# Performance work log

Hardware: AMD Instinct MI355X
Metric: run time of the kernel (lower is better)

The kernel has to match this reference:

```python
import jax, jax.numpy as jnp
import numpy as np

# batches, users-per-batch (max_user_num), servers-per-batch (max_server_num), dims
B, U, S, DU, DS, H = 64, 256, 64, 16, 16, 256
DEG_S, DEG_U = 8, 16
NU, NS = B * U, B * S
IN_DIM = U * DU + S * DS  # 5120


def setup_inputs() -> dict:
    key = jax.random.key(0)
    ks = jax.random.split(key, 12)
    x_user = jax.random.normal(ks[0], (NU, DU), jnp.float32)
    x_server = jax.random.normal(ks[1], (NS, DS), jnp.float32)
    # within-batch edges: user u in batch u//U connects to servers/users of same batch
    src_u2s = jnp.repeat(jnp.arange(NU), DEG_S)
    dst_u2s = (src_u2s // U) * S + jax.random.randint(ks[2], (NU * DEG_S,), 0, S)
    src_u2u = jnp.repeat(jnp.arange(NU), DEG_U)
    dst_u2u = (src_u2u // U) * U + jax.random.randint(ks[3], (NU * DEG_U,), 0, U)

    def lin(k, i, o):
        return jax.random.normal(k, (i, o), jnp.float32) * 0.02

    params = dict(
        oW1=lin(ks[4], IN_DIM, H), ob1=jnp.zeros((H,), jnp.float32),
        oW2=lin(ks[5], H, H), ob2=jnp.zeros((H,), jnp.float32),
        oW3=lin(ks[6], H, 2), ob3=jnp.zeros((2,), jnp.float32),
        sW1=lin(ks[7], IN_DIM, H), sb1=jnp.zeros((H,), jnp.float32),
        sW2=lin(ks[8], H, H), sb2=jnp.zeros((H,), jnp.float32),
        sW3=lin(ks[9], H, S), sb3=jnp.zeros((S,), jnp.float32),
    )
    return dict(x_user=x_user, x_server=x_server,
                src_u2s=src_u2s, dst_u2s=dst_u2s,
                src_u2u=src_u2u, dst_u2u=dst_u2u, **params)


def _mlp3(x, W1, b1, W2, b2, W3, b3):
    h = jax.nn.relu(x @ W1 + b1)
    h = jax.nn.sigmoid(h @ W2 + b2)
    return h @ W3 + b3


def reference(x_user, x_server, src_u2s, dst_u2s, src_u2u, dst_u2u,
              oW1, ob1, oW2, ob2, oW3, ob3, sW1, sb1, sW2, sb2, sW3, sb3):
    # scatter neighbor features into per-user dense observation slots
    # (edges are within-batch, so dst % S / dst % U is the local slot index,
    #  identical to the original global-offset scatter + batch mask)
    server_obs = (jnp.zeros((NU, S, DS), x_server.dtype)
                  .at[src_u2s, dst_u2s % S].set(x_server[dst_u2s]))
    user_obs = (jnp.zeros((NU, U, DU), x_user.dtype)
                .at[src_u2u, dst_u2u % U].set(x_user[dst_u2u]))
    feats = jnp.concatenate([server_obs.reshape(B, U, S * DS),
                             user_obs.reshape(B, U, U * DU)], axis=-1)  # [B,U,IN_DIM]
    offloading_probs = jax.nn.softmax(
        _mlp3(feats, oW1, ob1, oW2, ob2, oW3, ob3), axis=-1)  # [B,U,2]
    sel_logits = _mlp3(feats, sW1, sb1, sW2, sb2, sW3, sb3)   # [B,U,S]
    # -inf mask: 0 only at (user, server) pairs connected by a u2s edge
    non_probs = (jnp.full((NU, S), -jnp.inf, jnp.float32)
                 .at[src_u2s, dst_u2s % S].set(0.0)
                 .reshape(B, U, S))
    selection_probs = jax.nn.softmax(sel_logits + non_probs, axis=-1)
    return offloading_probs, selection_probs
```

## Files before the change

kernel.cpp:

```cpp
#include <hip/hip_runtime.h>
#include <hip/hip_bf16.h>
#include <math.h>
#include <cstdint>

#define NUSER 16384
#define BB    64
#define UU    256
#define SSLOT 64
#define HD    256
#define KTOT  320
#define DEGS  8
#define DEGU  16

typedef __attribute__((ext_vector_type(8))) short short8;
typedef __attribute__((ext_vector_type(4))) float f32x4;

static __device__ __forceinline__ __hip_bfloat16 f2b(float x) { return __float2bfloat16(x); }
static __device__ __forceinline__ unsigned pack2(float x, float y) {
  union { __hip_bfloat16 h[2]; unsigned u; } cv;
  cv.h[0] = f2b(x); cv.h[1] = f2b(y);
  return cv.u;
}

__global__ __launch_bounds__(256) void k_prep_pq(
    const int* __restrict__ dst_u2s, const int* __restrict__ dst_u2u,
    const float* __restrict__ oW2, const float* __restrict__ sW2,
    const float* __restrict__ sW3,
    const float* __restrict__ xu, const float* __restrict__ xs,
    const float* __restrict__ oW1, const float* __restrict__ sW1,
    unsigned long long* __restrict__ connS, unsigned* __restrict__ MSUW,
    __hip_bfloat16* __restrict__ W2T_o, __hip_bfloat16* __restrict__ W2T_s,
    __hip_bfloat16* __restrict__ W3T_s,
    __hip_bfloat16* __restrict__ P_o, __hip_bfloat16* __restrict__ P_s,
    __hip_bfloat16* __restrict__ Q_o, __hip_bfloat16* __restrict__ Q_s) {
  const int t = threadIdx.x;
  if (blockIdx.y == 0) {
    const int blk = blockIdx.x;
    if (blk < 64) {
      const int u = blk * 256 + t;
      unsigned long long ms = 0ull;
      #pragma unroll
      for (int i = 0; i < DEGS; ++i) ms |= 1ull << (dst_u2s[u * DEGS + i] & 63);
      connS[u] = ms;
      unsigned long long m0 = 0, m1 = 0, m2 = 0, m3 = 0;
      #pragma unroll
      for (int i = 0; i < DEGU; ++i) {
        int slot = dst_u2u[u * DEGU + i] & 255;
        unsigned long long bit = 1ull << (slot & 63);
        int w = slot >> 6;
        if (w == 0) m0 |= bit; else if (w == 1) m1 |= bit;
        else if (w == 2) m2 |= bit; else m3 |= bit;
      }
      unsigned* mw = MSUW + (size_t)u * 10;
      uint2* mw2 = (uint2*)mw;
      mw2[0] = make_uint2((unsigned)ms, (unsigned)(ms >> 32));
      mw2[1] = make_uint2((unsigned)m0, (unsigned)(m0 >> 32));
      mw2[2] = make_uint2((unsigned)m1, (unsigned)(m1 >> 32));
      mw2[3] = make_uint2((unsigned)m2, (unsigned)(m2 >> 32));
      mw2[4] = make_uint2((unsigned)m3, (unsigned)(m3 >> 32));
    } else {
      const int n = blk - 64;
      W2T_o[n * HD + t] = f2b(oW2[t * HD + n]);
      W2T_s[n * HD + t] = f2b(sW2[t * HD + n]);
      if (n < SSLOT) W3T_s[n * HD + t] = f2b(sW3[t * SSLOT + n]);
    }
    return;
  }
  const int wg = blockIdx.x;
  const int b0 = (blockIdx.y - 1) * 8;
  __shared__ float lx[8 * 16];
  const bool isS = wg < SSLOT;
  const int slot = isS ? wg : wg - SSLOT;
  if (t < 8 * 16) {
    int b = b0 + (t >> 4), d = t & 15;
    lx[t] = isS ? xs[(b * SSLOT + slot) * 16 + d] : xu[(b * UU + slot) * 16 + d];
  }
  __syncthreads();
  float wo[16], wsv[16];
  const int rbase = isS ? slot * 16 : SSLOT * 16 + slot * 16;
  #pragma unroll
  for (int d = 0; d < 16; ++d) {
    wo[d] = oW1[(rbase + d) * HD + t];
    wsv[d] = sW1[(rbase + d) * HD + t];
  }
  __hip_bfloat16* Ro = isS ? P_o : Q_o;
  __hip_bfloat16* Rs = isS ? P_s : Q_s;
  const int rows = isS ? SSLOT : UU;
  #pragma unroll
  for (int bi = 0; bi < 8; ++bi) {
    float ao = 0.f, as = 0.f;
    #pragma unroll
    for (int q = 0; q < 4; ++q) {
      float4 x4 = *(const float4*)&lx[bi * 16 + q * 4];
      ao = fmaf(x4.x, wo[q*4+0], ao); as = fmaf(x4.x, wsv[q*4+0], as);
      ao = fmaf(x4.y, wo[q*4+1], ao); as = fmaf(x4.y, wsv[q*4+1], as);
      ao = fmaf(x4.z, wo[q*4+2], ao); as = fmaf(x4.z, wsv[q*4+2], as);
      ao = fmaf(x4.w, wo[q*4+3], ao); as = fmaf(x4.w, wsv[q*4+3], as);
    }
    Ro[((b0 + bi) * rows + slot) * HD + t] = f2b(ao);
    Rs[((b0 + bi) * rows + slot) * HD + t] = f2b(as);
  }
}

__global__ __launch_bounds__(256) void k_tr(
    const __hip_bfloat16* __restrict__ P_o, const __hip_bfloat16* __restrict__ P_s,
    const __hip_bfloat16* __restrict__ Q_o, const __hip_bfloat16* __restrict__ Q_s,
    __hip_bfloat16* __restrict__ PQT_o, __hip_bfloat16* __restrict__ PQT_s) {
  const int b = blockIdx.x, mlp = blockIdx.y, nc = blockIdx.z;
  const int n0 = nc * 64;
  const int t = threadIdx.x;
  const __hip_bfloat16* P = mlp ? P_s : P_o;
  const __hip_bfloat16* Q = mlp ? Q_s : Q_o;
  __hip_bfloat16* PQT = mlp ? PQT_s : PQT_o;
  __shared__ __align__(16) short lds[64 * 72];
  for (int kt = 0; kt < 5; ++kt) {
    const __hip_bfloat16* src = (kt == 0) ? (P + (size_t)(b * SSLOT) * HD)
                                          : (Q + (size_t)(b * UU + (kt - 1) * 64) * HD);
    const int kout = (kt == 0) ? 0 : 64 + (kt - 1) * 64;
    #pragma unroll
    for (int i = 0; i < 2; ++i) {
      int c = t + i * 256;
      int row = c >> 3, cc = c & 7;
      *(short8*)&lds[row * 72 + cc * 8] =
          *(const short8*)(src + (size_t)row * HD + n0 + cc * 8);
    }
    __syncthreads();
    #pragma unroll
    for (int i = 0; i < 2; ++i) {
      int c = t + i * 256;
      int nrow = c >> 3, kc = c & 7;
      short8 v;
      #pragma unroll
      for (int e = 0; e < 8; ++e) v[e] = lds[(kc * 8 + e) * 72 + nrow];
      *(short8*)(PQT + (size_t)(b * 256 + n0 + nrow) * KTOT + kout + kc * 8) = v;
    }
    __syncthreads();
  }
}

__global__ __launch_bounds__(256) void k_h1(
    const unsigned* __restrict__ MSUW,
    const __hip_bfloat16* __restrict__ PQT_o, const __hip_bfloat16* __restrict__ PQT_s,
    const float* __restrict__ ob1, const float* __restrict__ sb1,
    __hip_bfloat16* __restrict__ h1o, __hip_bfloat16* __restrict__ h1s) {
  const int b = blockIdx.x >> 1, uh = blockIdx.x & 1;
  const int mlp = blockIdx.y, nh = blockIdx.z;
  const int n0 = nh * 128;
  const int t = threadIdx.x;
  const __hip_bfloat16* PQT = mlp ? PQT_s : PQT_o;
  const float* b1 = mlp ? sb1 : ob1;
  __hip_bfloat16* h1 = mlp ? h1s : h1o;

  __shared__ __align__(16) char smem[48128];
  short* pan = (short*)smem;
  unsigned* mskL = (unsigned*)(smem + 43008);

  {
    const unsigned* g = MSUW + (size_t)(b * 256 + uh * 128) * 10;
    #pragma unroll
    for (int i = 0; i < 5; ++i) mskL[t + 256 * i] = g[t + 256 * i];
  }
  const int lane = t & 63, w = t >> 6;
  const int lo = lane & 15, hi = lane >> 4;
  f32x4 acc[2][8] = {};
  for (int kc = 0; kc < 2; ++kc) {
    if (kc) __syncthreads();
    {
      const int r = t >> 1, c4 = t & 1;
      const __hip_bfloat16* src = PQT + (size_t)(b * 256 + n0 + r) * KTOT + kc * 160;
      #pragma unroll
      for (int i = 0; i < 10; ++i) {
        int cc = c4 + 2 * i;
        *(short8*)&pan[r * 168 + cc * 8] = *(const short8*)(src + cc * 8);
      }
    }
    __syncthreads();
    #pragma unroll
    for (int kt2 = 0; kt2 < 5; ++kt2) {
      const int kt = kc * 5 + kt2;
      short8 af[2], bf[8];
      #pragma unroll
      for (int rb = 0; rb < 2; ++rb) {
        int lu = w * 32 + rb * 16 + lo;
        unsigned m = mskL[lu * 10 + kt];
        unsigned by = (m >> (hi * 8)) & 0xFFu;
        union { unsigned u[4]; short8 s; } cv;
        cv.u[0] = ((by & 1u)  ? 0x3F80u : 0u) | ((by & 2u)   ? 0x3F800000u : 0u);
        cv.u[1] = ((by & 4u)  ? 0x3F80u : 0u) | ((by & 8u)   ? 0x3F800000u : 0u);
        cv.u[2] = ((by & 16u) ? 0x3F80u : 0u) | ((by & 32u)  ? 0x3F800000u : 0u);
        cv.u[3] = ((by & 64u) ? 0x3F80u : 0u) | ((by & 128u) ? 0x3F800000u : 0u);
        af[rb] = cv.s;
      }
      #pragma unroll
      for (int cb = 0; cb < 8; ++cb) {
        int n = cb * 16 + lo;
        bf[cb] = *(const short8*)&pan[n * 168 + (kt2 * 4 + hi) * 8];
      }
      #pragma unroll
      for (int rb = 0; rb < 2; ++rb)
        #pragma unroll
        for (int cb = 0; cb < 8; ++cb)
          acc[rb][cb] = __builtin_amdgcn_mfma_f32_16x16x32_bf16(af[rb], bf[cb], acc[rb][cb], 0, 0, 0);
    }
  }
  #pragma unroll
  for (int cb = 0; cb < 8; ++cb) {
    int n = cb * 16 + lo;
    float bv = b1[n0 + n];
    #pragma unroll
    for (int rb = 0; rb < 2; ++rb) {
      #pragma unroll
      for (int j = 0; j < 4; ++j) {
        int u = b * 256 + uh * 128 + w * 32 + rb * 16 + hi * 4 + j;
        h1[(size_t)u * HD + n0 + n] = f2b(fmaxf(acc[rb][cb][j] + bv, 0.f));
      }
    }
  }
}

__global__ __launch_bounds__(256) void k_heads(
    const __hip_bfloat16* __restrict__ h1o, const __hip_bfloat16* __restrict__ h1s,
    const __hip_bfloat16* __restrict__ W2T_o, const __hip_bfloat16* __restrict__ W2T_s,
    const float* __restrict__ ob2, const float* __restrict__ sb2,
    const float* __restrict__ oW3, const float* __restrict__ ob3,
    const __hip_bfloat16* __restrict__ W3T_s, const float* __restrict__ sb3,
    const unsigned long long* __restrict__ connS,
    float* __restrict__ out) {
  const int mlp = blockIdx.y;
  const int x = blockIdx.x;
  const int blk = (x & 7) * 32 + (x >> 3);
  const int u0 = blk * 64;
  const int t = threadIdx.x, lane = t & 63, wid = t >> 6;
  const int lo = lane & 15, hi = lane >> 4;

  const __hip_bfloat16* A   = mlp ? h1s : h1o;
  const __hip_bfloat16* W2T = mlp ? W2T_s : W2T_o;
  const float* b2 = mlp ? sb2 : ob2;

  __shared__ __align__(16) char lds[32768 + 36864];
  short* As = (short*)lds;
  short* Bs = (short*)(lds + 32768);
  float* part = (float*)lds;

  #pragma unroll
  for (int i = 0; i < 8; ++i) {
    int c = t + i * 256;
    int row = c >> 5, cc = c & 31;
    *(short8*)&As[row * 256 + (cc ^ (row & 7)) * 8] =
        *(const short8*)(A + (size_t)(u0 + row) * HD + cc * 8);
  }
  __syncthreads();

  f32x4 acc2[4][4] = {};
  for (int ks = 0; ks < 8; ++ks) {
    if (ks) __syncthreads();
    #pragma unroll
    for (int i = 0; i < 4; ++i) {
      int c = t + i * 256;
      int n = c >> 2, kc = c & 3;
      *(short8*)&Bs[n * 72 + kc * 8] =
          *(const short8*)(W2T + (size_t)n * HD + ks * 32 + kc * 8);
    }
    __syncthreads();
    short8 af[4], bf[4];
    #pragma unroll
    for (int rb = 0; rb < 4; ++rb) {
      int row = rb * 16 + lo;
      int ca = ks * 4 + hi;
      af[rb] = *(const short8*)&As[row * 256 + (ca ^ (row & 7)) * 8];
    }
    #pragma unroll
    for (int cb = 0; cb < 4; ++cb) {
      int n = wid * 64 + cb * 16 + lo;
      bf[cb] = *(const short8*)&Bs[n * 72 + hi * 8];
    }
    #pragma unroll
    for (int rb = 0; rb < 4; ++rb)
      #pragma unroll
      for (int cb = 0; cb < 4; ++cb)
        acc2[rb][cb] = __builtin_amdgcn_mfma_f32_16x16x32_bf16(af[rb], bf[cb], acc2[rb][cb], 0, 0, 0);
  }
  __syncthreads();

  if (mlp == 0) {
    float p0[4][4] = {}, p1[4][4] = {};
    #pragma unroll
    for (int cb = 0; cb < 4; ++cb) {
      int n = wid * 64 + cb * 16 + lo;
      float bs = b2[n], w0 = oW3[2 * n], w1 = oW3[2 * n + 1];
      #pragma unroll
      for (int rb = 0; rb < 4; ++rb)
        #pragma unroll
        for (int j = 0; j < 4; ++j) {
          float sig = 1.0f / (1.0f + __expf(-(acc2[rb][cb][j] + bs)));
          p0[rb][j] = fmaf(sig, w0, p0[rb][j]);
          p1[rb][j] = fmaf(sig, w1, p1[rb][j]);
        }
    }
    #pragma unroll
    for (int rb = 0; rb < 4; ++rb)
      #pragma unroll
      for (int j = 0; j < 4; ++j) {
        #pragma unroll
        for (int off = 1; off < 16; off <<= 1) {
          p0[rb][j] += __shfl_xor(p0[rb][j], off, 64);
          p1[rb][j] += __shfl_xor(p1[rb][j], off, 64);
        }
        if (lo == 0) {
          int row = rb * 16 + hi * 4 + j;
          part[wid * 128 + row * 2 + 0] = p0[rb][j];
          part[wid * 128 + row * 2 + 1] = p1[rb][j];
        }
      }
    __syncthreads();
    if (t < 64) {
      float q0 = part[t * 2] + part[128 + t * 2] + part[256 + t * 2] + part[384 + t * 2] + ob3[0];
      float q1 = part[t * 2 + 1] + part[128 + t * 2 + 1] + part[256 + t * 2 + 1] + part[384 + t * 2 + 1] + ob3[1];
      float m2 = fmaxf(q0, q1);
      float e0 = __expf(q0 - m2), e1 = __expf(q1 - m2);
      float iv = 1.0f / (e0 + e1);
      float2 r; r.x = e0 * iv; r.y = e1 * iv;
      *(float2*)(out + (size_t)(u0 + t) * 2) = r;
    }
  } else {
    short* sel = As;
    #pragma unroll
    for (int cb = 0; cb < 4; ++cb) {
      int n = wid * 64 + cb * 16 + lo;
      float bs = b2[n];
      #pragma unroll
      for (int rb = 0; rb < 4; ++rb)
        #pragma unroll
        for (int j = 0; j < 4; ++j) {
          int row = rb * 16 + hi * 4 + j;
          float sig = 1.0f / (1.0f + __expf(-(acc2[rb][cb][j] + bs)));
          sel[row * 256 + ((n >> 3) ^ (row & 7)) * 8 + (n & 7)] = (short)pack2(sig, 0.f);
        }
    }
    __syncthreads();
    f32x4 acc3[4] = {};
    #pragma unroll
    for (int ks = 0; ks < 8; ++ks) {
      int row = wid * 16 + lo;
      int ca = ks * 4 + hi;
      short8 af = *(const short8*)&sel[row * 256 + (ca ^ (row & 7)) * 8];
      #pragma unroll
      for (int cb = 0; cb < 4; ++cb) {
        short8 bf = *(const short8*)(W3T_s + (size_t)(cb * 16 + lo) * HD + ks * 32 + hi * 8);
        acc3[cb] = __builtin_amdgcn_mfma_f32_16x16x32_bf16(af, bf, acc3[cb], 0, 0, 0);
      }
    }
    float sb3n[4];
    #pragma unroll
    for (int cb = 0; cb < 4; ++cb) sb3n[cb] = sb3[cb * 16 + lo];
    const int ubase = u0 + wid * 16 + hi * 4;
    #pragma unroll
    for (int j = 0; j < 4; ++j) {
      unsigned long long m = connS[ubase + j];
      float v[4]; bool ok[4];
      float mx = -INFINITY;
      #pragma unroll
      for (int cb = 0; cb < 4; ++cb) {
        int n = cb * 16 + lo;
        ok[cb] = (m >> n) & 1ull;
        v[cb] = ok[cb] ? (acc3[cb][j] + sb3n[cb]) : -INFINITY;
        mx = fmaxf(mx, v[cb]);
      }
      #pragma unroll
      for (int off = 1; off < 16; off <<= 1) mx = fmaxf(mx, __shfl_xor(mx, off, 64));
      float e[4], ssum = 0.f;
      #pragma unroll
      for (int cb = 0; cb < 4; ++cb) {
        e[cb] = ok[cb] ? __expf(v[cb] - mx) : 0.f;
        ssum += e[cb];
      }
      #pragma unroll
      for (int off = 1; off < 16; off <<= 1) ssum += __shfl_xor(ssum, off, 64);
      float iv = 1.0f / ssum;
      #pragma unroll
      for (int cb = 0; cb < 4; ++cb) {
        int n = cb * 16 + lo;
        out[(size_t)NUSER * 2 + (size_t)(ubase + j) * SSLOT + n] = e[cb] * iv;
      }
    }
  }
}

extern "C" void kernel_launch(void* const* d_in, const int* in_sizes, int n_in,
                              void* d_out, int out_size, void* d_ws, size_t ws_size,
                              hipStream_t stream) {
  const float* x_user   = (const float*)d_in[0];
  const float* x_server = (const float*)d_in[1];
  const int*   dst_u2s  = (const int*)d_in[3];
  const int*   dst_u2u  = (const int*)d_in[5];
  const float* oW1 = (const float*)d_in[6];
  const float* ob1 = (const float*)d_in[7];
  const float* oW2 = (const float*)d_in[8];
  const float* ob2 = (const float*)d_in[9];
  const float* oW3 = (const float*)d_in[10];
  const float* ob3 = (const float*)d_in[11];
  const float* sW1 = (const float*)d_in[12];
  const float* sb1 = (const float*)d_in[13];
  const float* sW2 = (const float*)d_in[14];
  const float* sb2 = (const float*)d_in[15];
  const float* sW3 = (const float*)d_in[16];
  const float* sb3 = (const float*)d_in[17];

  char* ws = (char*)d_ws;
  unsigned long long* connS = (unsigned long long*)(ws + 0);
  unsigned*       MSUW  = (unsigned*)(ws + 131072);
  __hip_bfloat16* P_o  = (__hip_bfloat16*)(ws + 786432);
  __hip_bfloat16* P_s  = (__hip_bfloat16*)(ws + 2883584);
  __hip_bfloat16* Q_o  = (__hip_bfloat16*)(ws + 4980736);
  __hip_bfloat16* Q_s  = (__hip_bfloat16*)(ws + 13369344);
  __hip_bfloat16* PQT_o = (__hip_bfloat16*)(ws + 21757952);
  __hip_bfloat16* PQT_s = (__hip_bfloat16*)(ws + 32243712);
  __hip_bfloat16* h1o  = (__hip_bfloat16*)(ws + 42729472);
  __hip_bfloat16* h1s  = (__hip_bfloat16*)(ws + 51118080);
  __hip_bfloat16* W2T_o = (__hip_bfloat16*)(ws + 59506688);
  __hip_bfloat16* W2T_s = (__hip_bfloat16*)(ws + 59637760);
  __hip_bfloat16* W3T_s = (__hip_bfloat16*)(ws + 59768832);
  float* out = (float*)d_out;

  k_prep_pq<<<dim3(320, 9), 256, 0, stream>>>(
      dst_u2s, dst_u2u, oW2, sW2, sW3, x_user, x_server, oW1, sW1,
      connS, MSUW, W2T_o, W2T_s, W3T_s, P_o, P_s, Q_o, Q_s);
  k_tr<<<dim3(64, 2, 4), 256, 0, stream>>>(P_o, P_s, Q_o, Q_s, PQT_o, PQT_s);
  k_h1<<<dim3(128, 2, 2), 256, 0, stream>>>(MSUW, PQT_o, PQT_s, ob1, sb1, h1o, h1s);
  k_heads<<<dim3(256, 2), 256, 0, stream>>>(h1o, h1s, W2T_o, W2T_s, ob2, sb2,
                                            oW3, ob3, W3T_s, sb3, connS, out);
}
```

Baseline: 58.02 us.

## Pre-swizzle W2/W3 into MFMA fragment order and load B directly from global

The prep kernel now writes the second- and third-layer weights in a layout that matches the MFMA B-operand fragment per lane. The heads kernel then loads each B fragment with one contiguous 16-byte read from global or L2, instead of staging W2 tiles through LDS with two barriers per k-step. This removes the LDS staging, the barriers and about 36KB of shared memory per block, which may allow higher occupancy. In exchange every wave reads its weights from L2 rather than sharing them through LDS.

```diff
diff --git a/kernel.cpp b/kernel.cpp
--- a/kernel.cpp
+++ b/kernel.cpp
@@ -29,8 +29,8 @@
     const float* __restrict__ xu, const float* __restrict__ xs,
     const float* __restrict__ oW1, const float* __restrict__ sW1,
     unsigned long long* __restrict__ connS, unsigned* __restrict__ MSUW,
-    __hip_bfloat16* __restrict__ W2T_o, __hip_bfloat16* __restrict__ W2T_s,
-    __hip_bfloat16* __restrict__ W3T_s,
+    __hip_bfloat16* __restrict__ W2F_o, __hip_bfloat16* __restrict__ W2F_s,
+    __hip_bfloat16* __restrict__ W3F_s,
     __hip_bfloat16* __restrict__ P_o, __hip_bfloat16* __restrict__ P_s,
     __hip_bfloat16* __restrict__ Q_o, __hip_bfloat16* __restrict__ Q_s) {
   const int t = threadIdx.x;
@@ -58,11 +58,21 @@
       mw2[2] = make_uint2((unsigned)m1, (unsigned)(m1 >> 32));
       mw2[3] = make_uint2((unsigned)m2, (unsigned)(m2 >> 32));
       mw2[4] = make_uint2((unsigned)m3, (unsigned)(m3 >> 32));
+      {
+        const int n = blk;
+        const int ks = t >> 5, hi = (t >> 3) & 3, e = t & 7;
+        const int lane = hi * 16 + (n & 15);
+        const size_t idx = (size_t)((((n >> 4) * 8 + ks) * 64 + lane)) * 8 + e;
+        W3F_s[idx] = f2b(sW3[(ks * 32 + hi * 8 + e) * SSLOT + n]);
+      }
     } else {
       const int n = blk - 64;
-      W2T_o[n * HD + t] = f2b(oW2[t * HD + n]);
-      W2T_s[n * HD + t] = f2b(sW2[t * HD + n]);
-      if (n < SSLOT) W3T_s[n * HD + t] = f2b(sW3[t * SSLOT + n]);
+      const int ks = t >> 5, hi = (t >> 3) & 3, e = t & 7;
+      const int lane = hi * 16 + (n & 15);
+      const size_t idx = (size_t)((((n >> 4) * 8 + ks) * 64 + lane)) * 8 + e;
+      const int k = ks * 32 + hi * 8 + e;
+      W2F_o[idx] = f2b(oW2[k * HD + n]);
+      W2F_s[idx] = f2b(sW2[k * HD + n]);
     }
     return;
   }
@@ -220,10 +230,10 @@
 
 __global__ __launch_bounds__(256) void k_heads(
     const __hip_bfloat16* __restrict__ h1o, const __hip_bfloat16* __restrict__ h1s,
-    const __hip_bfloat16* __restrict__ W2T_o, const __hip_bfloat16* __restrict__ W2T_s,
+    const __hip_bfloat16* __restrict__ W2F_o, const __hip_bfloat16* __restrict__ W2F_s,
     const float* __restrict__ ob2, const float* __restrict__ sb2,
     const float* __restrict__ oW3, const float* __restrict__ ob3,
-    const __hip_bfloat16* __restrict__ W3T_s, const float* __restrict__ sb3,
+    const __hip_bfloat16* __restrict__ W3F_s, const float* __restrict__ sb3,
     const unsigned long long* __restrict__ connS,
     float* __restrict__ out) {
   const int mlp = blockIdx.y;
@@ -234,13 +244,12 @@
   const int lo = lane & 15, hi = lane >> 4;
 
   const __hip_bfloat16* A   = mlp ? h1s : h1o;
-  const __hip_bfloat16* W2T = mlp ? W2T_s : W2T_o;
+  const __hip_bfloat16* W2F = mlp ? W2F_s : W2F_o;
   const float* b2 = mlp ? sb2 : ob2;
 
-  __shared__ __align__(16) char lds[32768 + 36864];
+  __shared__ __align__(16) char lds[32768 + 2048];
   short* As = (short*)lds;
-  short* Bs = (short*)(lds + 32768);
-  float* part = (float*)lds;
+  float* part = (float*)(lds + 32768);
 
   #pragma unroll
   for (int i = 0; i < 8; ++i) {
@@ -252,16 +261,8 @@
   __syncthreads();
 
   f32x4 acc2[4][4] = {};
+  #pragma unroll
   for (int ks = 0; ks < 8; ++ks) {
-    if (ks) __syncthreads();
-    #pragma unroll
-    for (int i = 0; i < 4; ++i) {
-      int c = t + i * 256;
-      int n = c >> 2, kc = c & 3;
-      *(short8*)&Bs[n * 72 + kc * 8] =
-          *(const short8*)(W2T + (size_t)n * HD + ks * 32 + kc * 8);
-    }
-    __syncthreads();
     short8 af[4], bf[4];
     #pragma unroll
     for (int rb = 0; rb < 4; ++rb) {
@@ -271,8 +272,7 @@
     }
     #pragma unroll
     for (int cb = 0; cb < 4; ++cb) {
-      int n = wid * 64 + cb * 16 + lo;
-      bf[cb] = *(const short8*)&Bs[n * 72 + hi * 8];
+      bf[cb] = *(const short8*)(W2F + (size_t)((((wid * 4 + cb) * 8 + ks) * 64 + lane)) * 8);
     }
     #pragma unroll
     for (int rb = 0; rb < 4; ++rb)
@@ -346,7 +346,7 @@
       short8 af = *(const short8*)&sel[row * 256 + (ca ^ (row & 7)) * 8];
       #pragma unroll
       for (int cb = 0; cb < 4; ++cb) {
-        short8 bf = *(const short8*)(W3T_s + (size_t)(cb * 16 + lo) * HD + ks * 32 + hi * 8);
+        short8 bf = *(const short8*)(W3F_s + (size_t)(((cb * 8 + ks) * 64 + lane)) * 8);
         acc3[cb] = __builtin_amdgcn_mfma_f32_16x16x32_bf16(af, bf, acc3[cb], 0, 0, 0);
       }
     }
@@ -417,16 +417,16 @@
   __hip_bfloat16* PQT_s = (__hip_bfloat16*)(ws + 32243712);
   __hip_bfloat16* h1o  = (__hip_bfloat16*)(ws + 42729472);
   __hip_bfloat16* h1s  = (__hip_bfloat16*)(ws + 51118080);
-  __hip_bfloat16* W2T_o = (__hip_bfloat16*)(ws + 59506688);
-  __hip_bfloat16* W2T_s = (__hip_bfloat16*)(ws + 59637760);
-  __hip_bfloat16* W3T_s = (__hip_bfloat16*)(ws + 59768832);
+  __hip_bfloat16* W2F_o = (__hip_bfloat16*)(ws + 59506688);
+  __hip_bfloat16* W2F_s = (__hip_bfloat16*)(ws + 59637760);
+  __hip_bfloat16* W3F_s = (__hip_bfloat16*)(ws + 59768832);
   float* out = (float*)d_out;
 
   k_prep_pq<<<dim3(320, 9), 256, 0, stream>>>(
       dst_u2s, dst_u2u, oW2, sW2, sW3, x_user, x_server, oW1, sW1,
-      connS, MSUW, W2T_o, W2T_s, W3T_s, P_o, P_s, Q_o, Q_s);
+      connS, MSUW, W2F_o, W2F_s, W3F_s, P_o, P_s, Q_o, Q_s);
   k_tr<<<dim3(64, 2, 4), 256, 0, stream>>>(P_o, P_s, Q_o, Q_s, PQT_o, PQT_s);
   k_h1<<<dim3(128, 2, 2), 256, 0, stream>>>(MSUW, PQT_o, PQT_s, ob1, sb1, h1o, h1s);
-  k_heads<<<dim3(256, 2), 256, 0, stream>>>(h1o, h1s, W2T_o, W2T_s, ob2, sb2,
-                                            oW3, ob3, W3T_s, sb3, connS, out);
-}
+  k_heads<<<dim3(256, 2), 256, 0, stream>>>(h1o, h1s, W2F_o, W2F_s, ob2, sb2,
+                                            oW3, ob3, W3F_s, sb3, connS, out);
+}
```

After: 56.82 us (median of 2 runs). 1.02x faster.
